# Optimization experiments

Measured on AMD Instinct MI355X. Metric: run time of the kernel, lower is better.

## Reference

```python
import jax, jax.numpy as jnp
import numpy as np
import math

H, B, T = 4, 32, 1000
EPROJS, DUNITS, DK, DV = 1024, 1024, 512, 512
ACONV_CHANS, ACONV_FILTS = 100, 100
FILTS = [ACONV_FILTS * (h + 1) // H for h in range(H)]  # 25, 50, 75, 100


def setup_inputs() -> dict:
    key = jax.random.key(0)
    ks = jax.random.split(key, 16)
    s = 0.02  # small init to keep tanh unsaturated
    ap = jax.random.uniform(ks[3], (H, B, T), dtype=jnp.float32)
    ap = ap / ap.sum(-1, keepdims=True)  # previous attention weights (rows sum to 1)
    inp = {
        "enc_hs_pad": jax.random.normal(ks[0], (B, T, EPROJS), dtype=jnp.float32),
        "enc_hs_len": jnp.full((B,), T, dtype=jnp.int32),
        "dec_z": jax.random.normal(ks[1], (B, DUNITS), dtype=jnp.float32),
        "att_prev": ap,
        "Wq": jax.random.normal(ks[4], (H, DUNITS, DK), dtype=jnp.float32) * s,
        "bq": jnp.zeros((H, DK), dtype=jnp.float32),
        "Wk": jax.random.normal(ks[5], (H, EPROJS, DK), dtype=jnp.float32) * s,
        "Wv": jax.random.normal(ks[6], (H, EPROJS, DV), dtype=jnp.float32) * s,
        "g_w": jax.random.normal(ks[7], (H, DK), dtype=jnp.float32) * s,
        "g_b": jnp.zeros((H,), dtype=jnp.float32),
        "Watt": jax.random.normal(ks[8], (H, ACONV_CHANS, DK), dtype=jnp.float32) * s,
        "Wo": jax.random.normal(ks[9], (H * DV, EPROJS), dtype=jnp.float32) * s,
    }
    for h in range(H):
        inp[f"conv_w{h}"] = jax.random.normal(ks[10 + h], (ACONV_CHANS, 1, 2 * FILTS[h] + 1), dtype=jnp.float32) * s
    return inp


def _conv1d(x, w, f):
    # x: [B, T], w: [C, 1, K]; SAME padding like torch Conv2d(padding=(0, f)) -> [B, C, T]
    return jax.lax.conv_general_dilated(x[:, None, :], w, (1,), [(f, f)],
                                        dimension_numbers=("NCH", "OIH", "NCH"))


def reference(enc_hs_pad, enc_hs_len, dec_z, att_prev, Wq, bq, Wk, Wv, g_w, g_b,
              Watt, Wo, conv_w0, conv_w1, conv_w2, conv_w3):
    scaling = 1.0 / math.sqrt(DK)
    conv_ws = [conv_w0, conv_w1, conv_w2, conv_w3]
    # per-head K/V projections of encoder states: [H, B, T, dk/dv]
    k = jnp.einsum('btd,hde->hbte', enc_hs_pad, Wk)
    v = jnp.einsum('btd,hde->hbte', enc_hs_pad, Wv)
    # per-head query projection: [H, B, dk]
    q = jnp.einsum('bd,hde->hbe', dec_z, Wq) + bq[:, None, :]
    # location features: per-head conv (different filter widths) then linear -> [H, B, T, dk]
    att_conv = jnp.stack([_conv1d(att_prev[h], conv_ws[h], FILTS[h]).transpose(0, 2, 1)
                          for h in range(H)])  # [H, B, T, C]
    att_conv = jnp.einsum('hbtc,hce->hbte', att_conv, Watt)
    # energies via gvec: [H, B, T]
    e = jnp.einsum('hbte,he->hbt', jnp.tanh(k + att_conv + q[:, :, None, :]), g_w) + g_b[:, None, None]
    w = jax.nn.softmax(scaling * e, axis=-1)  # no length masking, as in the original
    # weighted sums per head, concatenated head-major: [B, H*dv]
    c = jnp.einsum('hbte,hbt->bhe', v, w).reshape(B, H * DV)
    out = c @ Wo  # [B, eprojs]
    return out, w
```

## Files before the change

### kernel.cpp

```cpp
#include <hip/hip_runtime.h>
#include <hip/hip_bf16.h>
#include <math.h>

#define Hh 4
#define Bb 32
#define Tt 1000
#define TP 1024
#define EPROJS_ 1024
#define DUNITS_ 1024
#define DKd 512
#define DVd 512
#define CC 100
#define KPAD 256
#define SCALING 0.04419417382415922f

typedef __attribute__((ext_vector_type(8))) short short8;
typedef __attribute__((ext_vector_type(4))) float floatx4;

__device__ __forceinline__ void async16(const void* g, void* l) {
    __builtin_amdgcn_global_load_lds(
        (const __attribute__((address_space(1))) unsigned int*)g,
        (__attribute__((address_space(3))) unsigned int*)l, 16, 0, 0);
}

__global__ __launch_bounds__(256) void enc_cvt_kernel(
    const float* __restrict__ enc, unsigned short* __restrict__ enc16)
{
    int t = blockIdx.x, b = blockIdx.y;
    int d = threadIdx.x * 4;
    float4 v = *(const float4*)(enc + ((size_t)(b * Tt + t)) * EPROJS_ + d);
    union { __hip_bfloat162 h2[2]; uint2 u; } u;
    u.h2[0] = __float22bfloat162_rn(make_float2(v.x, v.y));
    u.h2[1] = __float22bfloat162_rn(make_float2(v.z, v.w));
    *(uint2*)(enc16 + ((size_t)(b * TP + t)) * EPROJS_ + d) = u.u;
}

__global__ __launch_bounds__(256) void wkt_kernel(
    const float* __restrict__ Wk, unsigned short* __restrict__ Wkt)
{
    int et = blockIdx.x;
    int dt = blockIdx.y;
    int h  = blockIdx.z;
    __shared__ float tile[64][65];
    int tid = threadIdx.x;
    int r = tid >> 4, c4 = tid & 15;
    const float* src = Wk + ((size_t)(h * DUNITS_ + dt * 64)) * DKd + et * 64;
#pragma unroll
    for (int rr = 0; rr < 4; ++rr) {
        int row = r + rr * 16;
        *(float4*)&tile[row][c4 * 4] = *(const float4*)(src + (size_t)row * DKd + c4 * 4);
    }
    __syncthreads();
    unsigned short* dst = Wkt + ((size_t)(h * DKd + et * 64)) * EPROJS_ + dt * 64;
#pragma unroll
    for (int rr = 0; rr < 4; ++rr) {
        int el = r + rr * 16;
        union { __hip_bfloat162 h2[2]; uint2 u; } u;
        u.h2[0] = __float22bfloat162_rn(make_float2(tile[c4 * 4 + 0][el], tile[c4 * 4 + 1][el]));
        u.h2[1] = __float22bfloat162_rn(make_float2(tile[c4 * 4 + 2][el], tile[c4 * 4 + 3][el]));
        *(uint2*)(dst + (size_t)el * EPROJS_ + c4 * 4) = u.u;
    }
}

__global__ __launch_bounds__(256) void ww_kernel(
    const float* __restrict__ w0, const float* __restrict__ w1,
    const float* __restrict__ w2, const float* __restrict__ w3,
    const float* __restrict__ Watt, __hip_bfloat16* __restrict__ WWt)
{
    int k = blockIdx.x;
    int h = blockIdx.y;
    int f = 25 * (h + 1), Kh = 2 * f + 1;
    const float* cw = (h == 0) ? w0 : (h == 1) ? w1 : (h == 2) ? w2 : w3;
    int e = threadIdx.x;
    float acc0 = 0.f, acc1 = 0.f;
    if (k < Kh) {
        for (int c = 0; c < CC; ++c) {
            float wv = cw[c * Kh + k];
            acc0 += wv * Watt[(h * CC + c) * DKd + e];
            acc1 += wv * Watt[(h * CC + c) * DKd + e + 256];
        }
    }
    WWt[((size_t)(h * DKd + e)) * KPAD + k] = __float2bfloat16(acc0);
    WWt[((size_t)(h * DKd + e + 256)) * KPAD + k] = __float2bfloat16(acc1);
}

__global__ __launch_bounds__(256) void q_kernel(
    const float* __restrict__ dec_z, const float* __restrict__ Wq,
    float* __restrict__ q_buf)
{
    int et = blockIdx.x, kc = blockIdx.y, h = blockIdx.z;
    int d0 = kc * 64;
    __shared__ float zs[32][64];
    int tid = threadIdx.x;
    {
        int b = tid >> 3, dc = (tid & 7) * 8;
        const float* p = dec_z + (size_t)b * DUNITS_ + d0 + dc;
        *(float4*)&zs[b][dc] = *(const float4*)p;
        *(float4*)&zs[b][dc + 4] = *(const float4*)(p + 4);
    }
    __syncthreads();
    int e = et * 128 + (tid & 127);
    int dl0 = (tid >> 7) * 32;
    float wq[32];
#pragma unroll
    for (int dl = 0; dl < 32; ++dl)
        wq[dl] = Wq[((size_t)(h * DUNITS_ + d0 + dl0 + dl)) * DKd + e];
#pragma unroll
    for (int b = 0; b < 32; ++b) {
        float s = 0.f;
#pragma unroll
        for (int dl = 0; dl < 32; ++dl) s += zs[b][dl0 + dl] * wq[dl];
        atomicAdd(&q_buf[(h * Bb + b) * DKd + e], s);
    }
}

__global__ __launch_bounds__(256) void e_kernel(
    const unsigned short* __restrict__ enc16, const unsigned short* __restrict__ Wkt,
    const float* __restrict__ att_prev, const __hip_bfloat16* __restrict__ WWt,
    const float* __restrict__ q_buf, const float* __restrict__ bq,
    const float* __restrict__ g_w, float* __restrict__ e_buf)
{
    const int lin = blockIdx.x;
    const int xcd = lin & 7, pos = lin >> 3;
    const int b = (pos >> 7) * 8 + xcd;
    const int rem = pos & 127;
    const int h = rem >> 5;
    const int by = (rem & 31) >> 2;
    const int bx = rem & 3;
    const int t0 = by * 128, e0 = bx * 128;
    const int tid = threadIdx.x;
    const int lane = tid & 63, w = tid >> 6;
    const int wr = w >> 1, wc = w & 1;
    const int m = lane & 15, quad = lane >> 4;
    const int srow = tid >> 3;
    const int ko = (((tid & 7) ^ (srow & 7))) * 8;
    const int sw = m & 7;

    __shared__ __align__(16) short As[128 * 64];
    __shared__ __align__(16) short Bs[128 * 64];

    floatx4 acc[4][4];
#pragma unroll
    for (int i = 0; i < 4; ++i)
#pragma unroll
        for (int j = 0; j < 4; ++j) acc[i][j] = (floatx4){0.f, 0.f, 0.f, 0.f};

    const unsigned short* WkB = Wkt + ((size_t)(h * DKd + e0)) * EPROJS_;
    const unsigned short* encB = enc16 + ((size_t)(b * TP + t0)) * EPROJS_;
    char* AsDst = (char*)As + (tid & ~63) * 16;
    char* BsDst = (char*)Bs + (tid & ~63) * 16;

    for (int ch = 0; ch < 16; ++ch) {
        int d0 = ch * 64;
        __syncthreads();
#pragma unroll
        for (int it = 0; it < 4; ++it) {
            int r2 = it * 32 + srow;
            async16(encB + (size_t)r2 * EPROJS_ + d0 + ko, AsDst + it * 4096);
            async16(WkB + (size_t)r2 * EPROJS_ + d0 + ko, BsDst + it * 4096);
        }
        __syncthreads();
#pragma unroll
        for (int ks = 0; ks < 2; ++ks) {
            short8 af[4], bf[4];
#pragma unroll
            for (int i = 0; i < 4; ++i)
                af[i] = *(const short8*)&As[(wr * 64 + i * 16 + m) * 64 + (((ks << 2) + quad) ^ sw) * 8];
#pragma unroll
            for (int j = 0; j < 4; ++j)
                bf[j] = *(const short8*)&Bs[(wc * 64 + j * 16 + m) * 64 + (((ks << 2) + quad) ^ sw) * 8];
#pragma unroll
            for (int i = 0; i < 4; ++i)
#pragma unroll
                for (int j = 0; j < 4; ++j)
                    acc[i][j] = __builtin_amdgcn_mfma_f32_16x16x32_bf16(
                        af[i], bf[j], acc[i][j], 0, 0, 0);
        }
    }

    const int f = 25 * (h + 1);
    const int Kh = 2 * f + 1;
    const int nch2 = (Kh + 63) >> 6;
    const float* ab = att_prev + (size_t)(h * Bb + b) * Tt;
    const __hip_bfloat16* WWB = WWt + ((size_t)(h * DKd + e0)) * KPAD;
    for (int ch = 0; ch < nch2; ++ch) {
        int k0 = ch * 64;
        int ar = tid >> 1, half = tid & 1;
        int sbase = t0 + ar - f + k0 + half * 32;
        float v[32];
#pragma unroll
        for (int j2 = 0; j2 < 32; ++j2) {
            int s = sbase + j2;
            v[j2] = (s >= 0 && s < Tt) ? ab[s] : 0.f;
        }
        __syncthreads();
#pragma unroll
        for (int it = 0; it < 4; ++it) {
            int r2 = it * 32 + srow;
            async16(WWB + (size_t)r2 * KPAD + k0 + ko, BsDst + it * 4096);
        }
        union { short8 s[4]; __hip_bfloat162 hh[16]; } u;
#pragma unroll
        for (int j2 = 0; j2 < 16; ++j2)
            u.hh[j2] = __float22bfloat162_rn(make_float2(v[2 * j2], v[2 * j2 + 1]));
#pragma unroll
        for (int jj = 0; jj < 4; ++jj) {
            int phys = (half * 4 + jj) ^ (ar & 7);
            *(short8*)&As[ar * 64 + phys * 8] = u.s[jj];
        }
        __syncthreads();
#pragma unroll
        for (int ks = 0; ks < 2; ++ks) {
            short8 af[4], bf[4];
#pragma unroll
            for (int i = 0; i < 4; ++i)
                af[i] = *(const short8*)&As[(wr * 64 + i * 16 + m) * 64 + (((ks << 2) + quad) ^ sw) * 8];
#pragma unroll
            for (int j = 0; j < 4; ++j)
                bf[j] = *(const short8*)&Bs[(wc * 64 + j * 16 + m) * 64 + (((ks << 2) + quad) ^ sw) * 8];
#pragma unroll
            for (int i = 0; i < 4; ++i)
#pragma unroll
                for (int j = 0; j < 4; ++j)
                    acc[i][j] = __builtin_amdgcn_mfma_f32_16x16x32_bf16(
                        af[i], bf[j], acc[i][j], 0, 0, 0);
        }
    }

    const float* qrow = q_buf + (size_t)(h * Bb + b) * DKd;
    const float* bqrow = bq + h * DKd;
    const float* gwrow = g_w + h * DKd;
    float qv[4], gw[4];
#pragma unroll
    for (int j = 0; j < 4; ++j) {
        int e = e0 + wc * 64 + j * 16 + m;
        qv[j] = qrow[e] + bqrow[e];
        gw[j] = gwrow[e];
    }
    float* erow = e_buf + (size_t)(h * Bb + b) * Tt;
#pragma unroll
    for (int i = 0; i < 4; ++i) {
#pragma unroll
        for (int reg = 0; reg < 4; ++reg) {
            float s = 0.f;
#pragma unroll
            for (int j = 0; j < 4; ++j)
                s += tanhf(acc[i][j][reg] + qv[j]) * gw[j];
            s += __shfl_xor(s, 1);
            s += __shfl_xor(s, 2);
            s += __shfl_xor(s, 4);
            s += __shfl_xor(s, 8);
            int t = t0 + wr * 64 + i * 16 + quad * 4 + reg;
            if (m == 0 && t < Tt)
                atomicAdd(&erow[t], s);
        }
    }
}

__global__ __launch_bounds__(256) void softmax_kernel(
    const float* __restrict__ e_buf, float* __restrict__ wout)
{
    int rowid = blockIdx.x;
    const float* x = e_buf + rowid * Tt;
    float* y = wout + rowid * Tt;
    int tid = threadIdx.x;
    float v[4];
    float mx = -1e30f;
#pragma unroll
    for (int k = 0; k < 4; ++k) {
        int t = tid + k * 256;
        v[k] = (t < Tt) ? x[t] * SCALING : -1e30f;
        mx = fmaxf(mx, v[k]);
    }
    for (int off = 32; off >= 1; off >>= 1) mx = fmaxf(mx, __shfl_xor(mx, off));
    __shared__ float sm[4];
    __shared__ float ss[4];
    int wave = tid >> 6;
    if ((tid & 63) == 0) sm[wave] = mx;
    __syncthreads();
    mx = fmaxf(fmaxf(sm[0], sm[1]), fmaxf(sm[2], sm[3]));
    float s = 0.f;
#pragma unroll
    for (int k = 0; k < 4; ++k) {
        int t = tid + k * 256;
        v[k] = (t < Tt) ? __expf(v[k] - mx) : 0.f;
        s += v[k];
    }
    for (int off = 32; off >= 1; off >>= 1) s += __shfl_xor(s, off);
    if ((tid & 63) == 0) ss[wave] = s;
    __syncthreads();
    s = ss[0] + ss[1] + ss[2] + ss[3];
    float inv = 1.0f / s;
#pragma unroll
    for (int k = 0; k < 4; ++k) {
        int t = tid + k * 256;
        if (t < Tt) y[t] = v[k] * inv;
    }
}

__global__ __launch_bounds__(256) void ctx_kernel(
    const float* __restrict__ wout, const unsigned short* __restrict__ enc16,
    float* __restrict__ ctx)
{
    int dch = blockIdx.x;
    int b = blockIdx.y;
    int tq = blockIdx.z;
    int t0 = tq * 250;
    int tid = threadIdx.x;
    __shared__ float wl[4][252];
    __shared__ float red[8 * 4 * 128];
    for (int i = tid; i < 1000; i += 256) {
        int h = i / 250, tl = i - h * 250;
        wl[h][tl] = wout[(h * Bb + b) * Tt + t0 + tl];
    }
    __syncthreads();
    int g = tid >> 5, c = tid & 31;
    int d0 = dch * 128;
    float4 a[4];
#pragma unroll
    for (int h = 0; h < 4; ++h) a[h] = make_float4(0.f, 0.f, 0.f, 0.f);
    const unsigned short* encB = enc16 + (size_t)b * TP * EPROJS_ + d0 + c * 4;
    for (int t = t0 + g; t < t0 + 250; t += 8) {
        uint2 raw = *(const uint2*)(encB + (size_t)t * EPROJS_);
        float x0 = __uint_as_float(raw.x << 16);
        float x1 = __uint_as_float(raw.x & 0xffff0000u);
        float x2 = __uint_as_float(raw.y << 16);
        float x3 = __uint_as_float(raw.y & 0xffff0000u);
#pragma unroll
        for (int h = 0; h < 4; ++h) {
            float wv = wl[h][t - t0];
            a[h].x += wv * x0; a[h].y += wv * x1;
            a[h].z += wv * x2; a[h].w += wv * x3;
        }
    }
#pragma unroll
    for (int h = 0; h < 4; ++h)
        *(float4*)&red[((g * 4 + h) << 7) + c * 4] = a[h];
    __syncthreads();
    for (int i = tid; i < 512; i += 256) {
        int h = i >> 7, dd = i & 127;
        float ssum = 0.f;
#pragma unroll
        for (int g2 = 0; g2 < 8; ++g2) ssum += red[((g2 * 4 + h) << 7) + dd];
        atomicAdd(&ctx[(h * Bb + b) * EPROJS_ + d0 + dd], ssum);
    }
}

__global__ __launch_bounds__(256) void c_kernel(
    const float* __restrict__ ctx, const float* __restrict__ Wv,
    float* __restrict__ c_buf)
{
    int et = blockIdx.x, kc = blockIdx.y, h = blockIdx.z;
    int d0 = kc * 64;
    __shared__ float zs[32][64];
    int tid = threadIdx.x;
    {
        int b = tid >> 3, dc = (tid & 7) * 8;
        const float* p = ctx + ((size_t)(h * Bb + b)) * EPROJS_ + d0 + dc;
        *(float4*)&zs[b][dc] = *(const float4*)p;
        *(float4*)&zs[b][dc + 4] = *(const float4*)(p + 4);
    }
    __syncthreads();
    int e = et * 128 + (tid & 127);
    int dl0 = (tid >> 7) * 32;
    float wv[32];
#pragma unroll
    for (int dl = 0; dl < 32; ++dl)
        wv[dl] = Wv[((size_t)(h * EPROJS_ + d0 + dl0 + dl)) * DVd + e];
#pragma unroll
    for (int b = 0; b < 32; ++b) {
        float s = 0.f;
#pragma unroll
        for (int dl = 0; dl < 32; ++dl) s += zs[b][dl0 + dl] * wv[dl];
        atomicAdd(&c_buf[(h * Bb + b) * DVd + e], s);
    }
}

__global__ __launch_bounds__(256) void out_kernel(
    const float* __restrict__ c_buf, const float* __restrict__ Wo,
    float* __restrict__ outp)
{
    int ot = blockIdx.x;
    int kc = blockIdx.y;
    int k0 = kc * 64, o0 = ot * 128;
    __shared__ float cs[32][64];
    int tid = threadIdx.x;
    {
        int b = tid >> 3, k8 = (tid & 7) * 8;
        int h = k0 >> 9;
        const float* p = c_buf + ((size_t)(h * Bb + b)) * DVd + (k0 & 511) + k8;
        *(float4*)&cs[b][k8] = *(const float4*)p;
        *(float4*)&cs[b][k8 + 4] = *(const float4*)(p + 4);
    }
    __syncthreads();
    int o = o0 + (tid & 127);
    int kl0 = (tid >> 7) * 32;
    float wo[32];
#pragma unroll
    for (int kl = 0; kl < 32; ++kl)
        wo[kl] = Wo[((size_t)(k0 + kl0 + kl)) * EPROJS_ + o];
#pragma unroll
    for (int b = 0; b < 32; ++b) {
        float s = 0.f;
#pragma unroll
        for (int kl = 0; kl < 32; ++kl) s += cs[b][kl0 + kl] * wo[kl];
        atomicAdd(&outp[b * EPROJS_ + o], s);
    }
}

extern "C" void kernel_launch(void* const* d_in, const int* in_sizes, int n_in,
                              void* d_out, int out_size, void* d_ws, size_t ws_size,
                              hipStream_t stream) {
    const float* enc     = (const float*)d_in[0];
    const float* dec_z   = (const float*)d_in[2];
    const float* att_prev= (const float*)d_in[3];
    const float* Wq      = (const float*)d_in[4];
    const float* bq      = (const float*)d_in[5];
    const float* Wk      = (const float*)d_in[6];
    const float* Wv      = (const float*)d_in[7];
    const float* g_w     = (const float*)d_in[8];
    const float* Watt    = (const float*)d_in[10];
    const float* Wo      = (const float*)d_in[11];
    const float* cw0     = (const float*)d_in[12];
    const float* cw1     = (const float*)d_in[13];
    const float* cw2     = (const float*)d_in[14];
    const float* cw3     = (const float*)d_in[15];

    float* ws    = (float*)d_ws;
    float* q_buf = ws;
    float* e_buf = ws + 65536;
    float* c_buf = ws + 193536;
    float* ctx   = ws + 259072;
    unsigned short* enc16 = (unsigned short*)(ws + 390144);
    unsigned short* Wkt   = (unsigned short*)(ws + 17167360);
    __hip_bfloat16* WWt   = (__hip_bfloat16*)(ws + 18215936);
    float* outp  = (float*)d_out;
    float* wout  = outp + 32768;

    hipMemsetAsync(ws, 0, (size_t)390144 * sizeof(float), stream);
    hipMemsetAsync(d_out, 0, (size_t)32768 * sizeof(float), stream);

    enc_cvt_kernel<<<dim3(Tt, Bb), 256, 0, stream>>>(enc, enc16);
    wkt_kernel<<<dim3(8, 16, 4), 256, 0, stream>>>(Wk, Wkt);
    ww_kernel<<<dim3(KPAD, 4), 256, 0, stream>>>(cw0, cw1, cw2, cw3, Watt, WWt);
    q_kernel<<<dim3(4, 16, 4), 256, 0, stream>>>(dec_z, Wq, q_buf);
    e_kernel<<<4096, 256, 0, stream>>>(enc16, Wkt, att_prev, WWt,
                                       q_buf, bq, g_w, e_buf);
    softmax_kernel<<<128, 256, 0, stream>>>(e_buf, wout);
    ctx_kernel<<<dim3(8, 32, 4), 256, 0, stream>>>(wout, enc16, ctx);
    c_kernel<<<dim3(4, 16, 4), 256, 0, stream>>>(ctx, Wv, c_buf);
    out_kernel<<<dim3(8, 32), 256, 0, stream>>>(c_buf, Wo, outp);
}
```

Before: 568.3 us.

## Merge prep kernels, precompute bf16 conv windows, drop atomics and use fast tanh

Folds the encoder conversion, Wk transpose and conv-weight folding into one prep kernel. The same kernel also writes a padded bf16 im2col copy of att_prev, so the energy kernel can fetch the location-conv operand with async LDS loads instead of building it in registers. The tanh becomes an exp/rcp approximation. The q, c and out GEMVs become one-thread-per-output loops without atomics, ctx no longer splits over time, and the memsets are trimmed. This removes launch overhead, atomics and per-block conversion work, at the cost of a large extra workspace buffer and lower parallelism in the small GEMVs.

```diff
diff --git a/kernel.cpp b/kernel.cpp
--- a/kernel.cpp
+++ b/kernel.cpp
@@ -23,100 +23,122 @@
         (__attribute__((address_space(3))) unsigned int*)l, 16, 0, 0);
 }
 
-__global__ __launch_bounds__(256) void enc_cvt_kernel(
-    const float* __restrict__ enc, unsigned short* __restrict__ enc16)
-{
-    int t = blockIdx.x, b = blockIdx.y;
-    int d = threadIdx.x * 4;
-    float4 v = *(const float4*)(enc + ((size_t)(b * Tt + t)) * EPROJS_ + d);
-    union { __hip_bfloat162 h2[2]; uint2 u; } u;
-    u.h2[0] = __float22bfloat162_rn(make_float2(v.x, v.y));
-    u.h2[1] = __float22bfloat162_rn(make_float2(v.z, v.w));
-    *(uint2*)(enc16 + ((size_t)(b * TP + t)) * EPROJS_ + d) = u.u;
-}
-
-__global__ __launch_bounds__(256) void wkt_kernel(
-    const float* __restrict__ Wk, unsigned short* __restrict__ Wkt)
-{
-    int et = blockIdx.x;
-    int dt = blockIdx.y;
-    int h  = blockIdx.z;
-    __shared__ float tile[64][65];
-    int tid = threadIdx.x;
-    int r = tid >> 4, c4 = tid & 15;
-    const float* src = Wk + ((size_t)(h * DUNITS_ + dt * 64)) * DKd + et * 64;
-#pragma unroll
-    for (int rr = 0; rr < 4; ++rr) {
-        int row = r + rr * 16;
-        *(float4*)&tile[row][c4 * 4] = *(const float4*)(src + (size_t)row * DKd + c4 * 4);
-    }
-    __syncthreads();
-    unsigned short* dst = Wkt + ((size_t)(h * DKd + et * 64)) * EPROJS_ + dt * 64;
-#pragma unroll
-    for (int rr = 0; rr < 4; ++rr) {
-        int el = r + rr * 16;
-        union { __hip_bfloat162 h2[2]; uint2 u; } u;
-        u.h2[0] = __float22bfloat162_rn(make_float2(tile[c4 * 4 + 0][el], tile[c4 * 4 + 1][el]));
-        u.h2[1] = __float22bfloat162_rn(make_float2(tile[c4 * 4 + 2][el], tile[c4 * 4 + 3][el]));
-        *(uint2*)(dst + (size_t)el * EPROJS_ + c4 * 4) = u.u;
-    }
-}
-
-__global__ __launch_bounds__(256) void ww_kernel(
+__device__ __forceinline__ float fast_tanh(float x) {
+    float xc = fminf(fmaxf(x, -9.f), 9.f);
+    float p = __expf(2.f * xc);
+    return (p - 1.f) * __builtin_amdgcn_rcpf(p + 1.f);
+}
+
+__global__ __launch_bounds__(256) void prep_kernel(
+    const float* __restrict__ enc, const float* __restrict__ Wk,
     const float* __restrict__ w0, const float* __restrict__ w1,
     const float* __restrict__ w2, const float* __restrict__ w3,
-    const float* __restrict__ Watt, __hip_bfloat16* __restrict__ WWt)
-{
-    int k = blockIdx.x;
-    int h = blockIdx.y;
-    int f = 25 * (h + 1), Kh = 2 * f + 1;
-    const float* cw = (h == 0) ? w0 : (h == 1) ? w1 : (h == 2) ? w2 : w3;
-    int e = threadIdx.x;
-    float acc0 = 0.f, acc1 = 0.f;
-    if (k < Kh) {
-        for (int c = 0; c < CC; ++c) {
-            float wv = cw[c * Kh + k];
-            acc0 += wv * Watt[(h * CC + c) * DKd + e];
-            acc1 += wv * Watt[(h * CC + c) * DKd + e + 256];
-        }
-    }
-    WWt[((size_t)(h * DKd + e)) * KPAD + k] = __float2bfloat16(acc0);
-    WWt[((size_t)(h * DKd + e + 256)) * KPAD + k] = __float2bfloat16(acc1);
+    const float* __restrict__ Watt, const float* __restrict__ att_prev,
+    unsigned short* __restrict__ enc16, unsigned short* __restrict__ Wkt,
+    __hip_bfloat16* __restrict__ WWt, unsigned short* __restrict__ att2)
+{
+    __shared__ __align__(16) float smem[4160];
+    const int l = blockIdx.x;
+    const int tid = threadIdx.x;
+
+    if (l < 2048) {
+        int gtid = l * 256 + tid;
+        for (int i = gtid; i < 8192000; i += 524288) {
+            int b = i / 256000;
+            int rem = i - b * 256000;
+            int t = rem >> 8, d4 = rem & 255;
+            float4 v = *(const float4*)(enc + ((size_t)(b * Tt + t)) * EPROJS_ + d4 * 4);
+            union { __hip_bfloat162 h2[2]; uint2 u; } u;
+            u.h2[0] = __float22bfloat162_rn(make_float2(v.x, v.y));
+            u.h2[1] = __float22bfloat162_rn(make_float2(v.z, v.w));
+            *(uint2*)(enc16 + ((size_t)(b * TP + t)) * EPROJS_ + d4 * 4) = u.u;
+        }
+    } else if (l < 2560) {
+        int l2 = l - 2048;
+        int et = l2 & 7, dt = (l2 >> 3) & 15, h = l2 >> 7;
+        float (*tile)[65] = (float(*)[65])smem;
+        int r = tid >> 4, c4 = tid & 15;
+        const float* src = Wk + ((size_t)(h * DUNITS_ + dt * 64)) * DKd + et * 64;
+#pragma unroll
+        for (int rr = 0; rr < 4; ++rr) {
+            int row = r + rr * 16;
+            *(float4*)&tile[row][c4 * 4] = *(const float4*)(src + (size_t)row * DKd + c4 * 4);
+        }
+        __syncthreads();
+        unsigned short* dst = Wkt + ((size_t)(h * DKd + et * 64)) * EPROJS_ + dt * 64;
+#pragma unroll
+        for (int rr = 0; rr < 4; ++rr) {
+            int el = r + rr * 16;
+            union { __hip_bfloat162 h2[2]; uint2 u; } u;
+            u.h2[0] = __float22bfloat162_rn(make_float2(tile[c4 * 4 + 0][el], tile[c4 * 4 + 1][el]));
+            u.h2[1] = __float22bfloat162_rn(make_float2(tile[c4 * 4 + 2][el], tile[c4 * 4 + 3][el]));
+            *(uint2*)(dst + (size_t)el * EPROJS_ + c4 * 4) = u.u;
+        }
+    } else if (l < 3584) {
+        int l3 = l - 2560;
+        int k = l3 & 255, h = l3 >> 8;
+        int f = 25 * (h + 1), Kh = 2 * f + 1;
+        const float* cw = (h == 0) ? w0 : (h == 1) ? w1 : (h == 2) ? w2 : w3;
+        int e = tid;
+        float acc0 = 0.f, acc1 = 0.f;
+        if (k < Kh) {
+            for (int c = 0; c < CC; ++c) {
+                float wv = cw[c * Kh + k];
+                acc0 += wv * Watt[(h * CC + c) * DKd + e];
+                acc1 += wv * Watt[(h * CC + c) * DKd + e + 256];
+            }
+        }
+        WWt[((size_t)(h * DKd + e)) * KPAD + k] = __float2bfloat16(acc0);
+        WWt[((size_t)(h * DKd + e + 256)) * KPAD + k] = __float2bfloat16(acc1);
+    } else {
+        int l4 = l - 3584;
+        int h = l4 >> 8, b = (l4 >> 3) & 31, by = l4 & 7;
+        int f = 25 * (h + 1);
+        int Kpad = 64 * (h + 1);
+        int t0 = by * 128;
+        const float* ab = att_prev + (size_t)(h * Bb + b) * Tt;
+        float* win = smem;
+        int winlen = 127 + Kpad;
+        for (int i = tid; i < winlen; i += 256) {
+            int s = t0 - f + i;
+            win[i] = (s >= 0 && s < Tt) ? ab[s] : 0.f;
+        }
+        __syncthreads();
+        int a2off = 2097152 * ((h * (h + 1)) >> 1);
+        int r = tid >> 1, half = tid & 1;
+        unsigned short* dst = att2 + a2off + (size_t)(((b * 8 + by) * 128) + r) * Kpad;
+        int nst = Kpad >> 4;
+        for (int j = 0; j < nst; ++j) {
+            int k = half * (Kpad >> 1) + j * 8;
+            union { short8 s; __hip_bfloat162 hh[4]; } u;
+#pragma unroll
+            for (int q2 = 0; q2 < 4; ++q2)
+                u.hh[q2] = __float22bfloat162_rn(
+                    make_float2(win[r + k + 2 * q2], win[r + k + 2 * q2 + 1]));
+            *(short8*)(dst + k) = u.s;
+        }
+    }
 }
 
 __global__ __launch_bounds__(256) void q_kernel(
     const float* __restrict__ dec_z, const float* __restrict__ Wq,
     float* __restrict__ q_buf)
 {
-    int et = blockIdx.x, kc = blockIdx.y, h = blockIdx.z;
-    int d0 = kc * 64;
-    __shared__ float zs[32][64];
-    int tid = threadIdx.x;
-    {
-        int b = tid >> 3, dc = (tid & 7) * 8;
-        const float* p = dec_z + (size_t)b * DUNITS_ + d0 + dc;
-        *(float4*)&zs[b][dc] = *(const float4*)p;
-        *(float4*)&zs[b][dc + 4] = *(const float4*)(p + 4);
-    }
-    __syncthreads();
-    int e = et * 128 + (tid & 127);
-    int dl0 = (tid >> 7) * 32;
-    float wq[32];
-#pragma unroll
-    for (int dl = 0; dl < 32; ++dl)
-        wq[dl] = Wq[((size_t)(h * DUNITS_ + d0 + dl0 + dl)) * DKd + e];
-#pragma unroll
-    for (int b = 0; b < 32; ++b) {
-        float s = 0.f;
-#pragma unroll
-        for (int dl = 0; dl < 32; ++dl) s += zs[b][dl0 + dl] * wq[dl];
-        atomicAdd(&q_buf[(h * Bb + b) * DKd + e], s);
-    }
+    int col = blockIdx.x * 8 + (threadIdx.x & 7);
+    int b = threadIdx.x >> 3;
+    int h = col >> 9, e = col & 511;
+    const float* zp = dec_z + (size_t)b * DUNITS_;
+    const float* wp = Wq + (size_t)h * DUNITS_ * DKd + e;
+    float acc = 0.f;
+#pragma unroll 16
+    for (int k = 0; k < DUNITS_; ++k)
+        acc += zp[k] * wp[(size_t)k * DKd];
+    q_buf[(h * Bb + b) * DKd + e] = acc;
 }
 
 __global__ __launch_bounds__(256) void e_kernel(
     const unsigned short* __restrict__ enc16, const unsigned short* __restrict__ Wkt,
-    const float* __restrict__ att_prev, const __hip_bfloat16* __restrict__ WWt,
+    const unsigned short* __restrict__ att2, const __hip_bfloat16* __restrict__ WWt,
     const float* __restrict__ q_buf, const float* __restrict__ bq,
     const float* __restrict__ g_w, float* __restrict__ e_buf)
 {
@@ -178,35 +200,18 @@
         }
     }
 
-    const int f = 25 * (h + 1);
-    const int Kh = 2 * f + 1;
-    const int nch2 = (Kh + 63) >> 6;
-    const float* ab = att_prev + (size_t)(h * Bb + b) * Tt;
+    const int Kpad = 64 * (h + 1);
+    const int a2off = 2097152 * ((h * (h + 1)) >> 1);
+    const unsigned short* A2B = att2 + a2off + (size_t)((b * 8 + by) * 128) * Kpad;
     const __hip_bfloat16* WWB = WWt + ((size_t)(h * DKd + e0)) * KPAD;
-    for (int ch = 0; ch < nch2; ++ch) {
+    for (int ch = 0; ch <= h; ++ch) {
         int k0 = ch * 64;
-        int ar = tid >> 1, half = tid & 1;
-        int sbase = t0 + ar - f + k0 + half * 32;
-        float v[32];
-#pragma unroll
-        for (int j2 = 0; j2 < 32; ++j2) {
-            int s = sbase + j2;
-            v[j2] = (s >= 0 && s < Tt) ? ab[s] : 0.f;
-        }
         __syncthreads();
 #pragma unroll
         for (int it = 0; it < 4; ++it) {
             int r2 = it * 32 + srow;
+            async16(A2B + (size_t)r2 * Kpad + k0 + ko, AsDst + it * 4096);
             async16(WWB + (size_t)r2 * KPAD + k0 + ko, BsDst + it * 4096);
-        }
-        union { short8 s[4]; __hip_bfloat162 hh[16]; } u;
-#pragma unroll
-        for (int j2 = 0; j2 < 16; ++j2)
-            u.hh[j2] = __float22bfloat162_rn(make_float2(v[2 * j2], v[2 * j2 + 1]));
-#pragma unroll
-        for (int jj = 0; jj < 4; ++jj) {
-            int phys = (half * 4 + jj) ^ (ar & 7);
-            *(short8*)&As[ar * 64 + phys * 8] = u.s[jj];
         }
         __syncthreads();
 #pragma unroll
@@ -245,7 +250,7 @@
             float s = 0.f;
 #pragma unroll
             for (int j = 0; j < 4; ++j)
-                s += tanhf(acc[i][j][reg] + qv[j]) * gw[j];
+                s += fast_tanh(acc[i][j][reg] + qv[j]) * gw[j];
             s += __shfl_xor(s, 1);
             s += __shfl_xor(s, 2);
             s += __shfl_xor(s, 4);
@@ -304,14 +309,13 @@
 {
     int dch = blockIdx.x;
     int b = blockIdx.y;
-    int tq = blockIdx.z;
-    int t0 = tq * 250;
     int tid = threadIdx.x;
-    __shared__ float wl[4][252];
+    __shared__ float wl[4][1000];
     __shared__ float red[8 * 4 * 128];
-    for (int i = tid; i < 1000; i += 256) {
-        int h = i / 250, tl = i - h * 250;
-        wl[h][tl] = wout[(h * Bb + b) * Tt + t0 + tl];
+    for (int i = tid; i < 4000; i += 256) {
+        int h = i >> 10, tl = i & 1023;
+        h = i / 1000; tl = i - h * 1000;
+        wl[h][tl] = wout[(h * Bb + b) * Tt + tl];
     }
     __syncthreads();
     int g = tid >> 5, c = tid & 31;
@@ -320,7 +324,7 @@
 #pragma unroll
     for (int h = 0; h < 4; ++h) a[h] = make_float4(0.f, 0.f, 0.f, 0.f);
     const unsigned short* encB = enc16 + (size_t)b * TP * EPROJS_ + d0 + c * 4;
-    for (int t = t0 + g; t < t0 + 250; t += 8) {
+    for (int t = g; t < Tt; t += 8) {
         uint2 raw = *(const uint2*)(encB + (size_t)t * EPROJS_);
         float x0 = __uint_as_float(raw.x << 16);
         float x1 = __uint_as_float(raw.x & 0xffff0000u);
@@ -328,7 +332,7 @@
         float x3 = __uint_as_float(raw.y & 0xffff0000u);
 #pragma unroll
         for (int h = 0; h < 4; ++h) {
-            float wv = wl[h][t - t0];
+            float wv = wl[h][t];
             a[h].x += wv * x0; a[h].y += wv * x1;
             a[h].z += wv * x2; a[h].w += wv * x3;
         }
@@ -342,7 +346,7 @@
         float ssum = 0.f;
 #pragma unroll
         for (int g2 = 0; g2 < 8; ++g2) ssum += red[((g2 * 4 + h) << 7) + dd];
-        atomicAdd(&ctx[(h * Bb + b) * EPROJS_ + d0 + dd], ssum);
+        ctx[(h * Bb + b) * EPROJS_ + d0 + dd] = ssum;
     }
 }
 
@@ -350,62 +354,33 @@
     const float* __restrict__ ctx, const float* __restrict__ Wv,
     float* __restrict__ c_buf)
 {
-    int et = blockIdx.x, kc = blockIdx.y, h = blockIdx.z;
-    int d0 = kc * 64;
-    __shared__ float zs[32][64];
-    int tid = threadIdx.x;
-    {
-        int b = tid >> 3, dc = (tid & 7) * 8;
-        const float* p = ctx + ((size_t)(h * Bb + b)) * EPROJS_ + d0 + dc;
-        *(float4*)&zs[b][dc] = *(const float4*)p;
-        *(float4*)&zs[b][dc + 4] = *(const float4*)(p + 4);
-    }
-    __syncthreads();
-    int e = et * 128 + (tid & 127);
-    int dl0 = (tid >> 7) * 32;
-    float wv[32];
-#pragma unroll
-    for (int dl = 0; dl < 32; ++dl)
-        wv[dl] = Wv[((size_t)(h * EPROJS_ + d0 + dl0 + dl)) * DVd + e];
-#pragma unroll
-    for (int b = 0; b < 32; ++b) {
-        float s = 0.f;
-#pragma unroll
-        for (int dl = 0; dl < 32; ++dl) s += zs[b][dl0 + dl] * wv[dl];
-        atomicAdd(&c_buf[(h * Bb + b) * DVd + e], s);
-    }
+    int col = blockIdx.x * 8 + (threadIdx.x & 7);
+    int b = threadIdx.x >> 3;
+    int h = col >> 9, e = col & 511;
+    const float* xp = ctx + (size_t)(h * Bb + b) * EPROJS_;
+    const float* wp = Wv + (size_t)h * EPROJS_ * DVd + e;
+    float acc = 0.f;
+#pragma unroll 16
+    for (int k = 0; k < EPROJS_; ++k)
+        acc += xp[k] * wp[(size_t)k * DVd];
+    c_buf[(h * Bb + b) * DVd + e] = acc;
 }
 
 __global__ __launch_bounds__(256) void out_kernel(
     const float* __restrict__ c_buf, const float* __restrict__ Wo,
     float* __restrict__ outp)
 {
-    int ot = blockIdx.x;
-    int kc = blockIdx.y;
-    int k0 = kc * 64, o0 = ot * 128;
-    __shared__ float cs[32][64];
-    int tid = threadIdx.x;
-    {
-        int b = tid >> 3, k8 = (tid & 7) * 8;
-        int h = k0 >> 9;
-        const float* p = c_buf + ((size_t)(h * Bb + b)) * DVd + (k0 & 511) + k8;
-        *(float4*)&cs[b][k8] = *(const float4*)p;
-        *(float4*)&cs[b][k8 + 4] = *(const float4*)(p + 4);
-    }
-    __syncthreads();
-    int o = o0 + (tid & 127);
-    int kl0 = (tid >> 7) * 32;
-    float wo[32];
-#pragma unroll
-    for (int kl = 0; kl < 32; ++kl)
-        wo[kl] = Wo[((size_t)(k0 + kl0 + kl)) * EPROJS_ + o];
-#pragma unroll
-    for (int b = 0; b < 32; ++b) {
-        float s = 0.f;
-#pragma unroll
-        for (int kl = 0; kl < 32; ++kl) s += cs[b][kl0 + kl] * wo[kl];
-        atomicAdd(&outp[b * EPROJS_ + o], s);
-    }
+    int o = blockIdx.x * 8 + (threadIdx.x & 7);
+    int b = threadIdx.x >> 3;
+    const float* cp = c_buf + (size_t)b * DVd;
+    const float* wp = Wo + o;
+    float acc = 0.f;
+#pragma unroll 16
+    for (int k = 0; k < 2048; ++k) {
+        int h = k >> 9, e = k & 511;
+        acc += cp[(size_t)h * Bb * DVd + e] * wp[(size_t)k * EPROJS_];
+    }
+    outp[b * EPROJS_ + o] = acc;
 }
 
 extern "C" void kernel_launch(void* const* d_in, const int* in_sizes, int n_in,
@@ -434,20 +409,19 @@
     unsigned short* enc16 = (unsigned short*)(ws + 390144);
     unsigned short* Wkt   = (unsigned short*)(ws + 17167360);
     __hip_bfloat16* WWt   = (__hip_bfloat16*)(ws + 18215936);
+    unsigned short* att2  = (unsigned short*)(ws + 18478080);
     float* outp  = (float*)d_out;
     float* wout  = outp + 32768;
 
-    hipMemsetAsync(ws, 0, (size_t)390144 * sizeof(float), stream);
-    hipMemsetAsync(d_out, 0, (size_t)32768 * sizeof(float), stream);
-
-    enc_cvt_kernel<<<dim3(Tt, Bb), 256, 0, stream>>>(enc, enc16);
-    wkt_kernel<<<dim3(8, 16, 4), 256, 0, stream>>>(Wk, Wkt);
-    ww_kernel<<<dim3(KPAD, 4), 256, 0, stream>>>(cw0, cw1, cw2, cw3, Watt, WWt);
-    q_kernel<<<dim3(4, 16, 4), 256, 0, stream>>>(dec_z, Wq, q_buf);
-    e_kernel<<<4096, 256, 0, stream>>>(enc16, Wkt, att_prev, WWt,
+    hipMemsetAsync(e_buf, 0, (size_t)128000 * sizeof(float), stream);
+
+    prep_kernel<<<4608, 256, 0, stream>>>(enc, Wk, cw0, cw1, cw2, cw3, Watt,
+                                          att_prev, enc16, Wkt, WWt, att2);
+    q_kernel<<<256, 256, 0, stream>>>(dec_z, Wq, q_buf);
+    e_kernel<<<4096, 256, 0, stream>>>(enc16, Wkt, att2, WWt,
                                        q_buf, bq, g_w, e_buf);
     softmax_kernel<<<128, 256, 0, stream>>>(e_buf, wout);
-    ctx_kernel<<<dim3(8, 32, 4), 256, 0, stream>>>(wout, enc16, ctx);
-    c_kernel<<<dim3(4, 16, 4), 256, 0, stream>>>(ctx, Wv, c_buf);
-    out_kernel<<<dim3(8, 32), 256, 0, stream>>>(c_buf, Wo, outp);
-}
+    ctx_kernel<<<dim3(8, 32), 256, 0, stream>>>(wout, enc16, ctx);
+    c_kernel<<<256, 256, 0, stream>>>(ctx, Wv, c_buf);
+    out_kernel<<<128, 256, 0, stream>>>(c_buf, Wo, outp);
+}
```

Result: slower. 680.7 us (+19.8%).
